# Kernel optimization log

Measured on AMD Instinct MI355X. Metric: run time of the kernel, lower is better.

Reference implementation:

```python
import jax, jax.numpy as jnp
import numpy as np

B, T, D, U, R = 64, 512, 256, 256, 4


def setup_inputs() -> dict:
    key = jax.random.key(0)
    ks = jax.random.split(key, 12)
    inputs = jax.random.normal(ks[0], (B, T, D), dtype=jnp.float32)
    # per-timestep dependency indices into past timesteps; must satisfy dep[t] <= t
    dependencies = jnp.minimum(
        jax.random.randint(ks[1], (T, R - 1), 0, T), jnp.arange(T)[:, None]
    ).astype(jnp.int32)
    mask = jax.random.randint(ks[2], (B, T), 0, 2).astype(jnp.int32)
    initial_states = jax.random.normal(ks[3], (R, B, U), dtype=jnp.float32) * 0.1
    s = 1.0 / np.sqrt(U)
    def w(k, shape):
        return jax.random.normal(k, shape, dtype=jnp.float32) * s
    return dict(
        inputs=inputs, dependencies=dependencies, mask=mask, initial_states=initial_states,
        Wz=w(ks[4], (D, U)), Wr=w(ks[5], (D, U)), Wh=w(ks[6], (D, U)),
        Uz=w(ks[7], (U, U)), Ur=w(ks[8], (U, U)), Uh=w(ks[9], (U, U)),
        bz=jnp.zeros((U,), jnp.float32), br=jnp.zeros((U,), jnp.float32), bh=jnp.zeros((U,), jnp.float32),
    )


def reference(inputs, dependencies, mask, initial_states, Wz, Wr, Wh, Uz, Ur, Uh, bz, br, bh):
    Bn, Tn, _ = inputs.shape
    Rn = initial_states.shape[0]
    Un = Uz.shape[0]

    x = jnp.swapaxes(inputs, 0, 1)              # [T, B, D]  (time_major swap)
    m = jnp.swapaxes(mask, 0, 1).astype(bool)   # [T, B]
    # dependencies[i] is consumed AFTER step i (sets states for step i+1) -> shift by one
    dep_in = jnp.concatenate(
        [jnp.zeros((1, dependencies.shape[1]), dependencies.dtype), dependencies[:-1]], axis=0
    )

    def cell(x_t, states):
        # states: [R, B, U]  (child-sum Graph-GRU over recurrent_size predecessor states)
        r = jax.nn.sigmoid(x_t @ Wr + states @ Ur + br)          # [R, B, U]
        h_sum = states.sum(0)                                    # [B, U]
        z = jax.nn.sigmoid(x_t @ Wz + h_sum @ Uz + bz)
        h_tilde = jnp.tanh(x_t @ Wh + (r * states).sum(0) @ Uh + bh)
        h = z * (h_sum / Rn) + (1.0 - z) * h_tilde
        return h  # GRU: output == new state

    def step(carry, xs):
        prev_out, prev_state, buf, t = carry
        x_t, m_t, dep_t = xs
        gathered = buf[dep_t]                                    # [R-1, B, U] irregular history gather
        cand = jnp.concatenate([prev_state[None], gathered], axis=0)
        states = jnp.where(t == 0, initial_states, cand)
        h = cell(x_t, states)
        mt = m_t[:, None]                                        # [B, 1]
        out_m = jnp.where(mt, h, prev_out)                       # masked output (pre_output carry)
        st_m = jnp.where(mt, h, prev_state)                      # masked state  (pre_states carry)
        buf = buf.at[t].set(st_m)                                # successive_states[t]
        return (out_m, st_m, buf, t + 1), out_m

    carry0 = (
        jnp.zeros((Bn, Un), inputs.dtype),
        jnp.zeros((Bn, Un), inputs.dtype),
        jnp.zeros((Tn, Bn, Un), inputs.dtype),
        jnp.array(0, jnp.int32),
    )
    (last_out, last_state, _, _), outs = jax.lax.scan(step, carry0, (x, m, dep_in))

    # zero_output_for_mask
    last_out = jnp.where(m[-1][:, None], last_out, jnp.zeros_like(last_out))
    outs = jnp.where(m[:, :, None], outs, jnp.zeros_like(outs))
    outputs = jnp.swapaxes(outs, 0, 1)                           # back to [B, T, U]
    return outputs, last_out, last_state
```

## Files before the change

### kernel.cpp

```cpp
#include <hip/hip_runtime.h>
#include <cstdint>
#include <cstddef>

#define BN 64
#define TN 512
#define DN 256
#define UN 256
#define NC 768
#define SLOTS (TN + 5)
#define ZSLOT (TN + 4)

__device__ __forceinline__ float sigm(float x) {
  return 1.0f / (1.0f + __expf(-x));
}
__device__ __forceinline__ float tanh_fast(float x) {
  float e = __expf(-2.0f * x);
  return 2.0f / (1.0f + e) - 1.0f;
}

__global__ __launch_bounds__(256) void build_wcat(
    const float* __restrict__ Wr, const float* __restrict__ Wz, const float* __restrict__ Wh,
    const float* __restrict__ br, const float* __restrict__ bz, const float* __restrict__ bh,
    float* __restrict__ wcat, float* __restrict__ bias)
{
  int idx = blockIdx.x * 256 + threadIdx.x;
  if (idx < DN * NC) {
    int k = idx / NC, c = idx % NC;
    float v;
    if (c < 256)      v = Wr[k * UN + c];
    else if (c < 512) v = Wz[k * UN + (c - 256)];
    else              v = Wh[k * UN + (c - 512)];
    wcat[idx] = v;
  }
  if (idx < NC) {
    bias[idx] = (idx < 256) ? br[idx] : ((idx < 512) ? bz[idx - 256] : bh[idx - 512]);
  }
}

__global__ __launch_bounds__(256) void gemm_xw(
    const float* __restrict__ X, const float* __restrict__ Wc,
    const float* __restrict__ bias, float* __restrict__ P)
{
  __shared__ float As[32][68];
  __shared__ float Bs[32][64];
  const int tid = threadIdx.x;
  const int m0 = blockIdx.x * 64;
  const int n0 = blockIdx.y * 64;
  const int ty = tid >> 4, tx = tid & 15;
  float acc[4][4] = {};

  const int ar = tid >> 3;
  const int ak = (tid & 7) * 4;
  const int bk = tid >> 4;
  const int bn = (tid & 15) * 4;

  for (int k0 = 0; k0 < DN; k0 += 32) {
    float4 a0 = *(const float4*)(X + (size_t)(m0 + ar) * DN + k0 + ak);
    float4 a1 = *(const float4*)(X + (size_t)(m0 + 32 + ar) * DN + k0 + ak);
    As[ak + 0][ar] = a0.x; As[ak + 1][ar] = a0.y; As[ak + 2][ar] = a0.z; As[ak + 3][ar] = a0.w;
    As[ak + 0][32 + ar] = a1.x; As[ak + 1][32 + ar] = a1.y; As[ak + 2][32 + ar] = a1.z; As[ak + 3][32 + ar] = a1.w;
    *(float4*)&Bs[bk][bn]      = *(const float4*)(Wc + (size_t)(k0 + bk) * NC + n0 + bn);
    *(float4*)&Bs[bk + 16][bn] = *(const float4*)(Wc + (size_t)(k0 + bk + 16) * NC + n0 + bn);
    __syncthreads();
#pragma unroll
    for (int kk = 0; kk < 32; kk++) {
      float4 av = *(const float4*)&As[kk][ty * 4];
      float4 bv = *(const float4*)&Bs[kk][tx * 4];
      acc[0][0] += av.x * bv.x; acc[0][1] += av.x * bv.y; acc[0][2] += av.x * bv.z; acc[0][3] += av.x * bv.w;
      acc[1][0] += av.y * bv.x; acc[1][1] += av.y * bv.y; acc[1][2] += av.y * bv.z; acc[1][3] += av.y * bv.w;
      acc[2][0] += av.z * bv.x; acc[2][1] += av.z * bv.y; acc[2][2] += av.z * bv.z; acc[2][3] += av.z * bv.w;
      acc[3][0] += av.w * bv.x; acc[3][1] += av.w * bv.y; acc[3][2] += av.w * bv.z; acc[3][3] += av.w * bv.w;
    }
    __syncthreads();
  }
  float4 bb = *(const float4*)(bias + n0 + tx * 4);
#pragma unroll
  for (int i = 0; i < 4; i++) {
    float4 o;
    o.x = acc[i][0] + bb.x; o.y = acc[i][1] + bb.y;
    o.z = acc[i][2] + bb.z; o.w = acc[i][3] + bb.w;
    *(float4*)(P + (size_t)(m0 + ty * 4 + i) * NC + n0 + tx * 4) = o;
  }
}

__global__ __launch_bounds__(1024, 4) void recurrent_kernel(
    const float* __restrict__ P,
    const float* __restrict__ Ur, const float* __restrict__ Uz, const float* __restrict__ Uh,
    const int* __restrict__ dep, const int* __restrict__ mask,
    const float* __restrict__ init,
    float* __restrict__ out,
    float* __restrict__ buf_s, float* __restrict__ buf_pr, float* __restrict__ buf_pz)
{
  const int b = blockIdx.x;
  const int tid = threadIdx.x;
  const int g = tid >> 8;
  const int u = tid & 255;
  const int qd = tid >> 6;
  const int cd = (tid & 63) * 4;

  float wh[64];
  {
    const float* p2 = Uh + (size_t)(64 * g) * UN + u;
#pragma unroll
    for (int kk = 0; kk < 64; kk++) {
      wh[kk] = p2[(size_t)kk * UN];
    }
  }

  __shared__ float ls[4][256], lpr[4][256], lpz[4][256];
  __shared__ float lx[NC];
  __shared__ float rs[256], hs[256], zv[256], hv[256];
  __shared__ float red0[4][256];
  __shared__ float reddR[16][256], reddZ[16][256];
  __shared__ float scur[256], prcur[256], pzcur[256];
  __shared__ int eff[TN];
  __shared__ int mloc[TN];
  __shared__ int deploc[TN * 3];

  for (int i = tid; i < TN; i += 1024) mloc[i] = mask[b * TN + i];
  for (int i = tid; i < TN * 3; i += 1024) deploc[i] = dep[i];

  const size_t bufBase = (size_t)b * SLOTS * UN;

  {
    float v = init[((size_t)g * BN + b) * UN + u];
    ls[g][u] = v;
    buf_s[bufBase + (size_t)(TN + g) * UN + u] = v;
    if (tid < 256) {
      scur[u] = 0.0f; prcur[u] = 0.0f; pzcur[u] = 0.0f;
      buf_s[bufBase + (size_t)ZSLOT * UN + u] = 0.0f;
      buf_pr[bufBase + (size_t)ZSLOT * UN + u] = 0.0f;
      buf_pz[bufBase + (size_t)ZSLOT * UN + u] = 0.0f;
    }
  }
  __syncthreads();

#pragma unroll 1
  for (int gg = 0; gg < 4; gg++) {
    float4 arA = {0, 0, 0, 0}, azA = {0, 0, 0, 0};
    const float* bR = Ur + (size_t)(qd * 16) * UN + cd;
    const float* bZ = Uz + (size_t)(qd * 16) * UN + cd;
#pragma unroll 4
    for (int kk = 0; kk < 16; kk++) {
      float hk = ls[gg][qd * 16 + kk];
      float4 w1 = *(const float4*)(bR + (size_t)kk * UN);
      float4 w2 = *(const float4*)(bZ + (size_t)kk * UN);
      arA.x = fmaf(hk, w1.x, arA.x); arA.y = fmaf(hk, w1.y, arA.y);
      arA.z = fmaf(hk, w1.z, arA.z); arA.w = fmaf(hk, w1.w, arA.w);
      azA.x = fmaf(hk, w2.x, azA.x); azA.y = fmaf(hk, w2.y, azA.y);
      azA.z = fmaf(hk, w2.z, azA.z); azA.w = fmaf(hk, w2.w, azA.w);
    }
    *(float4*)&reddR[qd][cd] = arA;
    *(float4*)&reddZ[qd][cd] = azA;
    __syncthreads();
    if (tid < 256) {
      float prn = 0.0f, pzn = 0.0f;
#pragma unroll
      for (int q = 0; q < 16; q++) { prn += reddR[q][tid]; pzn += reddZ[q][tid]; }
      buf_pr[bufBase + (size_t)(TN + gg) * UN + tid] = prn;
      buf_pz[bufBase + (size_t)(TN + gg) * UN + tid] = pzn;
    }
    __syncthreads();
  }

  const size_t outB = (size_t)b * TN * UN;
  const size_t pB = (size_t)b * TN * NC;

#pragma unroll 1
  for (int t = 0; t < TN; t++) {
    const int m = mloc[t];
    if (m == 0) {
      if (tid < 256) out[outB + (size_t)t * UN + u] = 0.0f;
      if (tid == 0) eff[t] = (t == 0) ? ZSLOT : eff[t - 1];
      __syncthreads();
      continue;
    }
    if (t > 0 && g == 0) {
      ls[0][u] = scur[u]; lpr[0][u] = prcur[u]; lpz[0][u] = pzcur[u];
    } else {
      int src = (t == 0) ? (TN + g) : eff[deploc[(t - 1) * 3 + (g - 1)]];
      size_t base = bufBase + (size_t)src * UN + u;
      ls[g][u]  = buf_s[base];
      lpr[g][u] = buf_pr[base];
      lpz[g][u] = buf_pz[base];
    }
    if (tid < NC) lx[tid] = P[pB + (size_t)t * NC + tid];
    __syncthreads();
    if (tid < 256) {
      float s0 = ls[0][u], s1 = ls[1][u], s2 = ls[2][u], s3 = ls[3][u];
      float xr = lx[u];
      float r0 = sigm(xr + lpr[0][u]);
      float r1 = sigm(xr + lpr[1][u]);
      float r2 = sigm(xr + lpr[2][u]);
      float r3 = sigm(xr + lpr[3][u]);
      rs[u] = r0 * s0 + r1 * s1 + r2 * s2 + r3 * s3;
      hs[u] = (s0 + s1) + (s2 + s3);
      zv[u] = sigm(lx[256 + u] + ((lpz[0][u] + lpz[1][u]) + (lpz[2][u] + lpz[3][u])));
    }
    __syncthreads();
    {
      float a0 = 0, a1 = 0, a2 = 0, a3 = 0;
      const float4* v4 = (const float4*)&rs[64 * g];
#pragma unroll
      for (int kk = 0; kk < 16; kk++) {
        float4 v = v4[kk];
        a0 += v.x * wh[4 * kk];     a1 += v.y * wh[4 * kk + 1];
        a2 += v.z * wh[4 * kk + 2]; a3 += v.w * wh[4 * kk + 3];
      }
      red0[g][u] = (a0 + a1) + (a2 + a3);
    }
    __syncthreads();
    if (tid < 256) {
      float ht = tanh_fast(lx[512 + u] + ((red0[0][u] + red0[1][u]) + (red0[2][u] + red0[3][u])));
      float z = zv[u];
      float h = z * hs[u] * 0.25f + (1.0f - z) * ht;
      hv[u] = h; scur[u] = h;
      out[outB + (size_t)t * UN + u] = h;
    }
    __syncthreads();
    {
      float4 arA = {0, 0, 0, 0}, azA = {0, 0, 0, 0};
      const float* bR = Ur + (size_t)(qd * 16) * UN + cd;
      const float* bZ = Uz + (size_t)(qd * 16) * UN + cd;
#pragma unroll 4
      for (int kk = 0; kk < 16; kk++) {
        float hk = hv[qd * 16 + kk];
        float4 w1 = *(const float4*)(bR + (size_t)kk * UN);
        float4 w2 = *(const float4*)(bZ + (size_t)kk * UN);
        arA.x = fmaf(hk, w1.x, arA.x); arA.y = fmaf(hk, w1.y, arA.y);
        arA.z = fmaf(hk, w1.z, arA.z); arA.w = fmaf(hk, w1.w, arA.w);
        azA.x = fmaf(hk, w2.x, azA.x); azA.y = fmaf(hk, w2.y, azA.y);
        azA.z = fmaf(hk, w2.z, azA.z); azA.w = fmaf(hk, w2.w, azA.w);
      }
      *(float4*)&reddR[qd][cd] = arA;
      *(float4*)&reddZ[qd][cd] = azA;
    }
    __syncthreads();
    if (tid < 256) {
      float prn = 0.0f, pzn = 0.0f;
#pragma unroll
      for (int q = 0; q < 16; q++) { prn += reddR[q][tid]; pzn += reddZ[q][tid]; }
      prcur[tid] = prn; pzcur[tid] = pzn;
      size_t base = bufBase + (size_t)t * UN + tid;
      buf_s[base]  = hv[tid];
      buf_pr[base] = prn;
      buf_pz[base] = pzn;
    }
    if (tid == 0) eff[t] = t;
    __syncthreads();
  }

  if (tid < 256) {
    float lst = scur[u];
    out[(size_t)BN * TN * UN + (size_t)b * UN + u] = mloc[TN - 1] ? lst : 0.0f;
    out[(size_t)BN * TN * UN + (size_t)BN * UN + (size_t)b * UN + u] = lst;
  }
}

extern "C" void kernel_launch(void* const* d_in, const int* in_sizes, int n_in,
                              void* d_out, int out_size, void* d_ws, size_t ws_size,
                              hipStream_t stream) {
  const float* inputs       = (const float*)d_in[0];
  const int*   dependencies = (const int*)d_in[1];
  const int*   mask         = (const int*)d_in[2];
  const float* initial      = (const float*)d_in[3];
  const float* Wz = (const float*)d_in[4];
  const float* Wr = (const float*)d_in[5];
  const float* Wh = (const float*)d_in[6];
  const float* Uz = (const float*)d_in[7];
  const float* Ur = (const float*)d_in[8];
  const float* Uh = (const float*)d_in[9];
  const float* bz = (const float*)d_in[10];
  const float* br = (const float*)d_in[11];
  const float* bh = (const float*)d_in[12];

  float* out = (float*)d_out;
  float* ws  = (float*)d_ws;
  float* wcat    = ws;
  float* bias    = wcat + (size_t)DN * NC;
  float* precomp = bias + NC;
  float* buf_s   = precomp + (size_t)BN * TN * NC;
  float* buf_pr  = buf_s + (size_t)BN * SLOTS * UN;
  float* buf_pz  = buf_pr + (size_t)BN * SLOTS * UN;

  build_wcat<<<(DN * NC + 255) / 256, 256, 0, stream>>>(Wr, Wz, Wh, br, bz, bh, wcat, bias);
  gemm_xw<<<dim3(BN * TN / 64, NC / 64), 256, 0, stream>>>(inputs, wcat, bias, precomp);
  recurrent_kernel<<<BN, 1024, 0, stream>>>(precomp, Ur, Uz, Uh, dependencies, mask, initial,
                                            out, buf_s, buf_pr, buf_pz);
}
```

Baseline: 2.062 ms.

## Halve recurrent block size and keep Ur/Uz slices in registers and LDS

Shrinks the recurrent kernel from 1024 to 512 threads and gives each thread twice as many Uh weights in registers. Part of each wave's Ur/Uz slice now lives in registers and part in shared memory, and only the remainder is streamed from global memory each step. The eff table is precomputed once by a single thread, so masked steps no longer need a barrier. This targets per-step global weight loads and barrier count, at the cost of much higher register pressure and fewer threads per step.

```diff
diff --git a/kernel.cpp b/kernel.cpp
--- a/kernel.cpp
+++ b/kernel.cpp
@@ -9,6 +9,11 @@
 #define NC 768
 #define SLOTS (TN + 5)
 #define ZSLOT (TN + 4)
+
+#define NT 512
+#define RREG 8
+#define RLDS 6
+#define RSTR 18
 
 __device__ __forceinline__ float sigm(float x) {
   return 1.0f / (1.0f + __expf(-x));
@@ -83,7 +88,7 @@
   }
 }
 
-__global__ __launch_bounds__(1024, 4) void recurrent_kernel(
+__global__ __launch_bounds__(NT, 2) void recurrent_kernel(
     const float* __restrict__ P,
     const float* __restrict__ Ur, const float* __restrict__ Uz, const float* __restrict__ Uh,
     const int* __restrict__ dep, const int* __restrict__ mask,
@@ -93,39 +98,65 @@
 {
   const int b = blockIdx.x;
   const int tid = threadIdx.x;
-  const int g = tid >> 8;
+  const int g2 = tid >> 8;
   const int u = tid & 255;
-  const int qd = tid >> 6;
-  const int cd = (tid & 63) * 4;
-
-  float wh[64];
+  const int wv = tid >> 6;
+  const int lane = tid & 63;
+  const int c4 = lane * 4;
+
+  float wh[128];
   {
-    const float* p2 = Uh + (size_t)(64 * g) * UN + u;
-#pragma unroll
-    for (int kk = 0; kk < 64; kk++) {
+    const float* p2 = Uh + (size_t)(128 * g2) * UN + u;
+#pragma unroll
+    for (int kk = 0; kk < 128; kk++) {
       wh[kk] = p2[(size_t)kk * UN];
     }
   }
-
+  float4 wrgR[RREG], wrgZ[RREG];
+  {
+    const float4* pR = (const float4*)Ur + (size_t)(32 * wv) * 64 + lane;
+    const float4* pZ = (const float4*)Uz + (size_t)(32 * wv) * 64 + lane;
+#pragma unroll
+    for (int r = 0; r < RREG; r++) {
+      wrgR[r] = pR[(size_t)r * 64];
+      wrgZ[r] = pZ[(size_t)r * 64];
+    }
+  }
+
+  __shared__ float4 wlds[2 * RLDS * 8 * 64];
   __shared__ float ls[4][256], lpr[4][256], lpz[4][256];
   __shared__ float lx[NC];
-  __shared__ float rs[256], hs[256], zv[256], hv[256];
-  __shared__ float red0[4][256];
-  __shared__ float reddR[16][256], reddZ[16][256];
+  __shared__ float rs[256], hs[256], zv[256];
+  __shared__ float red0[2][256];
+  __shared__ float redd2[2][8][256];
   __shared__ float scur[256], prcur[256], pzcur[256];
   __shared__ int eff[TN];
   __shared__ int mloc[TN];
   __shared__ int deploc[TN * 3];
 
-  for (int i = tid; i < TN; i += 1024) mloc[i] = mask[b * TN + i];
-  for (int i = tid; i < TN * 3; i += 1024) deploc[i] = dep[i];
+  {
+    const float4* pR = (const float4*)Ur + (size_t)(32 * wv + RREG) * 64 + lane;
+    const float4* pZ = (const float4*)Uz + (size_t)(32 * wv + RREG) * 64 + lane;
+#pragma unroll
+    for (int r = 0; r < RLDS; r++) {
+      wlds[((0 * RLDS + r) * 8 + wv) * 64 + lane] = pR[(size_t)r * 64];
+      wlds[((1 * RLDS + r) * 8 + wv) * 64 + lane] = pZ[(size_t)r * 64];
+    }
+  }
+
+  for (int i = tid; i < TN; i += NT) mloc[i] = mask[b * TN + i];
+  for (int i = tid; i < TN * 3; i += NT) deploc[i] = dep[i];
 
   const size_t bufBase = (size_t)b * SLOTS * UN;
 
   {
-    float v = init[((size_t)g * BN + b) * UN + u];
-    ls[g][u] = v;
-    buf_s[bufBase + (size_t)(TN + g) * UN + u] = v;
+#pragma unroll
+    for (int gi = 0; gi < 2; gi++) {
+      int gg = gi * 2 + g2;
+      float v = init[((size_t)gg * BN + b) * UN + u];
+      ls[gg][u] = v;
+      buf_s[bufBase + (size_t)(TN + gg) * UN + u] = v;
+    }
     if (tid < 256) {
       scur[u] = 0.0f; prcur[u] = 0.0f; pzcur[u] = 0.0f;
       buf_s[bufBase + (size_t)ZSLOT * UN + u] = 0.0f;
@@ -135,28 +166,56 @@
   }
   __syncthreads();
 
+  if (tid == 0) {
+    int e = ZSLOT;
+    for (int t2 = 0; t2 < TN; t2++) { if (mloc[t2]) e = t2; eff[t2] = e; }
+  }
+
+  auto proj2 = [&](const float* hsrc) {
+    float4 aR = {0, 0, 0, 0}, aZ = {0, 0, 0, 0};
+    const float* hb = hsrc + 32 * wv;
+#pragma unroll
+    for (int r = 0; r < RREG; r++) {
+      float hk = hb[r];
+      aR.x = fmaf(hk, wrgR[r].x, aR.x); aR.y = fmaf(hk, wrgR[r].y, aR.y);
+      aR.z = fmaf(hk, wrgR[r].z, aR.z); aR.w = fmaf(hk, wrgR[r].w, aR.w);
+      aZ.x = fmaf(hk, wrgZ[r].x, aZ.x); aZ.y = fmaf(hk, wrgZ[r].y, aZ.y);
+      aZ.z = fmaf(hk, wrgZ[r].z, aZ.z); aZ.w = fmaf(hk, wrgZ[r].w, aZ.w);
+    }
+#pragma unroll
+    for (int r = 0; r < RLDS; r++) {
+      float hk = hb[RREG + r];
+      float4 w0 = wlds[((0 * RLDS + r) * 8 + wv) * 64 + lane];
+      float4 w1 = wlds[((1 * RLDS + r) * 8 + wv) * 64 + lane];
+      aR.x = fmaf(hk, w0.x, aR.x); aR.y = fmaf(hk, w0.y, aR.y);
+      aR.z = fmaf(hk, w0.z, aR.z); aR.w = fmaf(hk, w0.w, aR.w);
+      aZ.x = fmaf(hk, w1.x, aZ.x); aZ.y = fmaf(hk, w1.y, aZ.y);
+      aZ.z = fmaf(hk, w1.z, aZ.z); aZ.w = fmaf(hk, w1.w, aZ.w);
+    }
+    const float4* pR = (const float4*)Ur + (size_t)(32 * wv + RREG + RLDS) * 64 + lane;
+    const float4* pZ = (const float4*)Uz + (size_t)(32 * wv + RREG + RLDS) * 64 + lane;
+#pragma unroll 6
+    for (int r = 0; r < RSTR; r++) {
+      float hk = hb[RREG + RLDS + r];
+      float4 w0 = pR[(size_t)r * 64];
+      float4 w1 = pZ[(size_t)r * 64];
+      aR.x = fmaf(hk, w0.x, aR.x); aR.y = fmaf(hk, w0.y, aR.y);
+      aR.z = fmaf(hk, w0.z, aR.z); aR.w = fmaf(hk, w0.w, aR.w);
+      aZ.x = fmaf(hk, w1.x, aZ.x); aZ.y = fmaf(hk, w1.y, aZ.y);
+      aZ.z = fmaf(hk, w1.z, aZ.z); aZ.w = fmaf(hk, w1.w, aZ.w);
+    }
+    *(float4*)&redd2[0][wv][c4] = aR;
+    *(float4*)&redd2[1][wv][c4] = aZ;
+  };
+
 #pragma unroll 1
   for (int gg = 0; gg < 4; gg++) {
-    float4 arA = {0, 0, 0, 0}, azA = {0, 0, 0, 0};
-    const float* bR = Ur + (size_t)(qd * 16) * UN + cd;
-    const float* bZ = Uz + (size_t)(qd * 16) * UN + cd;
-#pragma unroll 4
-    for (int kk = 0; kk < 16; kk++) {
-      float hk = ls[gg][qd * 16 + kk];
-      float4 w1 = *(const float4*)(bR + (size_t)kk * UN);
-      float4 w2 = *(const float4*)(bZ + (size_t)kk * UN);
-      arA.x = fmaf(hk, w1.x, arA.x); arA.y = fmaf(hk, w1.y, arA.y);
-      arA.z = fmaf(hk, w1.z, arA.z); arA.w = fmaf(hk, w1.w, arA.w);
-      azA.x = fmaf(hk, w2.x, azA.x); azA.y = fmaf(hk, w2.y, azA.y);
-      azA.z = fmaf(hk, w2.z, azA.z); azA.w = fmaf(hk, w2.w, azA.w);
-    }
-    *(float4*)&reddR[qd][cd] = arA;
-    *(float4*)&reddZ[qd][cd] = azA;
+    proj2(ls[gg]);
     __syncthreads();
     if (tid < 256) {
       float prn = 0.0f, pzn = 0.0f;
 #pragma unroll
-      for (int q = 0; q < 16; q++) { prn += reddR[q][tid]; pzn += reddZ[q][tid]; }
+      for (int q = 0; q < 8; q++) { prn += redd2[0][q][tid]; pzn += redd2[1][q][tid]; }
       buf_pr[bufBase + (size_t)(TN + gg) * UN + tid] = prn;
       buf_pz[bufBase + (size_t)(TN + gg) * UN + tid] = pzn;
     }
@@ -171,20 +230,22 @@
     const int m = mloc[t];
     if (m == 0) {
       if (tid < 256) out[outB + (size_t)t * UN + u] = 0.0f;
-      if (tid == 0) eff[t] = (t == 0) ? ZSLOT : eff[t - 1];
-      __syncthreads();
       continue;
     }
-    if (t > 0 && g == 0) {
-      ls[0][u] = scur[u]; lpr[0][u] = prcur[u]; lpz[0][u] = pzcur[u];
-    } else {
-      int src = (t == 0) ? (TN + g) : eff[deploc[(t - 1) * 3 + (g - 1)]];
-      size_t base = bufBase + (size_t)src * UN + u;
-      ls[g][u]  = buf_s[base];
-      lpr[g][u] = buf_pr[base];
-      lpz[g][u] = buf_pz[base];
-    }
-    if (tid < NC) lx[tid] = P[pB + (size_t)t * NC + tid];
+#pragma unroll
+    for (int gi = 0; gi < 2; gi++) {
+      int gg = gi * 2 + g2;
+      if (t > 0 && gg == 0) {
+        ls[0][u] = scur[u]; lpr[0][u] = prcur[u]; lpz[0][u] = pzcur[u];
+      } else {
+        int src = (t == 0) ? (TN + gg) : eff[deploc[(t - 1) * 3 + (gg - 1)]];
+        size_t base = bufBase + (size_t)src * UN + u;
+        ls[gg][u]  = buf_s[base];
+        lpr[gg][u] = buf_pr[base];
+        lpz[gg][u] = buf_pz[base];
+      }
+    }
+    for (int i = tid; i < NC; i += NT) lx[i] = P[pB + (size_t)t * NC + i];
     __syncthreads();
     if (tid < 256) {
       float s0 = ls[0][u], s1 = ls[1][u], s2 = ls[2][u], s3 = ls[3][u];
@@ -200,53 +261,36 @@
     __syncthreads();
     {
       float a0 = 0, a1 = 0, a2 = 0, a3 = 0;
-      const float4* v4 = (const float4*)&rs[64 * g];
-#pragma unroll
-      for (int kk = 0; kk < 16; kk++) {
+      const float4* v4 = (const float4*)&rs[128 * g2];
+#pragma unroll
+      for (int kk = 0; kk < 32; kk++) {
         float4 v = v4[kk];
         a0 += v.x * wh[4 * kk];     a1 += v.y * wh[4 * kk + 1];
         a2 += v.z * wh[4 * kk + 2]; a3 += v.w * wh[4 * kk + 3];
       }
-      red0[g][u] = (a0 + a1) + (a2 + a3);
-    }
-    __syncthreads();
-    if (tid < 256) {
-      float ht = tanh_fast(lx[512 + u] + ((red0[0][u] + red0[1][u]) + (red0[2][u] + red0[3][u])));
+      red0[g2][u] = (a0 + a1) + (a2 + a3);
+    }
+    __syncthreads();
+    if (tid < 256) {
+      float ht = tanh_fast(lx[512 + u] + (red0[0][u] + red0[1][u]));
       float z = zv[u];
       float h = z * hs[u] * 0.25f + (1.0f - z) * ht;
-      hv[u] = h; scur[u] = h;
+      scur[u] = h;
       out[outB + (size_t)t * UN + u] = h;
     }
     __syncthreads();
-    {
-      float4 arA = {0, 0, 0, 0}, azA = {0, 0, 0, 0};
-      const float* bR = Ur + (size_t)(qd * 16) * UN + cd;
-      const float* bZ = Uz + (size_t)(qd * 16) * UN + cd;
-#pragma unroll 4
-      for (int kk = 0; kk < 16; kk++) {
-        float hk = hv[qd * 16 + kk];
-        float4 w1 = *(const float4*)(bR + (size_t)kk * UN);
-        float4 w2 = *(const float4*)(bZ + (size_t)kk * UN);
-        arA.x = fmaf(hk, w1.x, arA.x); arA.y = fmaf(hk, w1.y, arA.y);
-        arA.z = fmaf(hk, w1.z, arA.z); arA.w = fmaf(hk, w1.w, arA.w);
-        azA.x = fmaf(hk, w2.x, azA.x); azA.y = fmaf(hk, w2.y, azA.y);
-        azA.z = fmaf(hk, w2.z, azA.z); azA.w = fmaf(hk, w2.w, azA.w);
-      }
-      *(float4*)&reddR[qd][cd] = arA;
-      *(float4*)&reddZ[qd][cd] = azA;
-    }
+    proj2(scur);
     __syncthreads();
     if (tid < 256) {
       float prn = 0.0f, pzn = 0.0f;
 #pragma unroll
-      for (int q = 0; q < 16; q++) { prn += reddR[q][tid]; pzn += reddZ[q][tid]; }
+      for (int q = 0; q < 8; q++) { prn += redd2[0][q][tid]; pzn += redd2[1][q][tid]; }
       prcur[tid] = prn; pzcur[tid] = pzn;
       size_t base = bufBase + (size_t)t * UN + tid;
-      buf_s[base]  = hv[tid];
+      buf_s[base]  = scur[tid];
       buf_pr[base] = prn;
       buf_pz[base] = pzn;
     }
-    if (tid == 0) eff[t] = t;
     __syncthreads();
   }
 
@@ -285,6 +329,6 @@
 
   build_wcat<<<(DN * NC + 255) / 256, 256, 0, stream>>>(Wr, Wz, Wh, br, bz, bh, wcat, bias);
   gemm_xw<<<dim3(BN * TN / 64, NC / 64), 256, 0, stream>>>(inputs, wcat, bias, precomp);
-  recurrent_kernel<<<BN, 1024, 0, stream>>>(precomp, Ur, Uz, Uh, dependencies, mask, initial,
-                                            out, buf_s, buf_pr, buf_pz);
-}
+  recurrent_kernel<<<BN, NT, 0, stream>>>(precomp, Ur, Uz, Uh, dependencies, mask, initial,
+                                          out, buf_s, buf_pr, buf_pz);
+}
```

Measured after the change: 2.184 ms. 1.06x slower.

## Split each batch recurrence across four cooperating blocks with global flag sync

Applied to the files above, without the earlier changes.

The recurrent kernel now uses four 512-thread blocks per batch element, each owning a 64-column slice of the hidden state. Its slice of Ur/Uz is kept in shared memory instead of being re-read from global memory every step. The blocks swap their r*s and h slices through global memory using release/acquire flags and spin-waits, twice per active timestep. Masked-out steps now skip all work and barriers, and the effective-slot table is precomputed. This spreads work over more CUs and cuts global weight traffic, at the cost of cross-block synchronisation latency and a reliance on all 256 blocks being co-resident to avoid deadlock.

```diff
diff --git a/kernel.cpp b/kernel.cpp
--- a/kernel.cpp
+++ b/kernel.cpp
@@ -9,6 +9,8 @@
 #define NC 768
 #define SLOTS (TN + 5)
 #define ZSLOT (TN + 4)
+#define JW 4
+#define NT 512
 
 __device__ __forceinline__ float sigm(float x) {
   return 1.0f / (1.0f + __expf(-x));
@@ -21,7 +23,8 @@
 __global__ __launch_bounds__(256) void build_wcat(
     const float* __restrict__ Wr, const float* __restrict__ Wz, const float* __restrict__ Wh,
     const float* __restrict__ br, const float* __restrict__ bz, const float* __restrict__ bh,
-    float* __restrict__ wcat, float* __restrict__ bias)
+    float* __restrict__ wcat, float* __restrict__ bias,
+    int* __restrict__ flagA, int* __restrict__ flagB)
 {
   int idx = blockIdx.x * 256 + threadIdx.x;
   if (idx < DN * NC) {
@@ -35,6 +38,7 @@
   if (idx < NC) {
     bias[idx] = (idx < 256) ? br[idx] : ((idx < 512) ? bz[idx - 256] : bh[idx - 512]);
   }
+  if (idx < BN * JW) { flagA[idx] = 0; flagB[idx] = 0; }
 }
 
 __global__ __launch_bounds__(256) void gemm_xw(
@@ -83,177 +87,218 @@
   }
 }
 
-__global__ __launch_bounds__(1024, 4) void recurrent_kernel(
+__global__ __launch_bounds__(NT, 1) void recurrent_kernel(
     const float* __restrict__ P,
     const float* __restrict__ Ur, const float* __restrict__ Uz, const float* __restrict__ Uh,
     const int* __restrict__ dep, const int* __restrict__ mask,
     const float* __restrict__ init,
     float* __restrict__ out,
-    float* __restrict__ buf_s, float* __restrict__ buf_pr, float* __restrict__ buf_pz)
+    float* __restrict__ buf_s, float* __restrict__ buf_pr, float* __restrict__ buf_pz,
+    float* __restrict__ xrs, int* flagA, int* flagB)
 {
-  const int b = blockIdx.x;
+  const int bj = blockIdx.x;
+  const int b = bj & (BN - 1);
+  const int j = bj >> 6;
+  const int col0 = j * 64;
   const int tid = threadIdx.x;
-  const int g = tid >> 8;
-  const int u = tid & 255;
-  const int qd = tid >> 6;
-  const int cd = (tid & 63) * 4;
-
-  float wh[64];
+  const int c = tid & 63;
+
+  const int kg8 = tid >> 6;
+  float wh[32];
   {
-    const float* p2 = Uh + (size_t)(64 * g) * UN + u;
-#pragma unroll
-    for (int kk = 0; kk < 64; kk++) {
-      wh[kk] = p2[(size_t)kk * UN];
-    }
-  }
-
-  __shared__ float ls[4][256], lpr[4][256], lpz[4][256];
-  __shared__ float lx[NC];
-  __shared__ float rs[256], hs[256], zv[256], hv[256];
-  __shared__ float red0[4][256];
-  __shared__ float reddR[16][256], reddZ[16][256];
-  __shared__ float scur[256], prcur[256], pzcur[256];
+    const float* pu = Uh + (size_t)(32 * kg8) * UN + col0 + c;
+#pragma unroll
+    for (int kk = 0; kk < 32; kk++) wh[kk] = pu[(size_t)kk * UN];
+  }
+
+  __shared__ float4 wrz[2][256][16];
+  __shared__ float hfull[256];
+  __shared__ float rfull[256];
+  __shared__ float ls[4][64], lpr[4][64], lpz[4][64];
+  __shared__ float lx[3][64];
+  __shared__ float rsl[64], hsl[64], zvl[64];
+  __shared__ float redB[8][64];
+  __shared__ float redd[2][16][64];
+  __shared__ float scur[64], prcur[64], pzcur[64];
   __shared__ int eff[TN];
   __shared__ int mloc[TN];
   __shared__ int deploc[TN * 3];
 
-  for (int i = tid; i < TN; i += 1024) mloc[i] = mask[b * TN + i];
-  for (int i = tid; i < TN * 3; i += 1024) deploc[i] = dep[i];
-
-  const size_t bufBase = (size_t)b * SLOTS * UN;
-
-  {
-    float v = init[((size_t)g * BN + b) * UN + u];
-    ls[g][u] = v;
-    buf_s[bufBase + (size_t)(TN + g) * UN + u] = v;
-    if (tid < 256) {
-      scur[u] = 0.0f; prcur[u] = 0.0f; pzcur[u] = 0.0f;
-      buf_s[bufBase + (size_t)ZSLOT * UN + u] = 0.0f;
-      buf_pr[bufBase + (size_t)ZSLOT * UN + u] = 0.0f;
-      buf_pz[bufBase + (size_t)ZSLOT * UN + u] = 0.0f;
-    }
-  }
+  for (int i = tid; i < 2 * 256 * 16; i += NT) {
+    int mat = i >> 12, k = (i >> 4) & 255, ch = i & 15;
+    const float* src = mat ? Uz : Ur;
+    wrz[mat][k][ch] = *(const float4*)(src + (size_t)k * UN + col0 + ch * 4);
+  }
+  for (int i = tid; i < TN; i += NT) mloc[i] = mask[b * TN + i];
+  for (int i = tid; i < TN * 3; i += NT) deploc[i] = dep[i];
+  if (tid < 64) { scur[c] = 0.0f; prcur[c] = 0.0f; pzcur[c] = 0.0f; }
   __syncthreads();
+
+  if (tid == 0) {
+    int e = ZSLOT;
+    for (int t2 = 0; t2 < TN; t2++) { if (mloc[t2]) e = t2; eff[t2] = e; }
+  }
+
+  const size_t bufS = (size_t)b * SLOTS * UN;
+  const size_t bufP = (size_t)(b * JW + j) * SLOTS * 64;
 
 #pragma unroll 1
   for (int gg = 0; gg < 4; gg++) {
-    float4 arA = {0, 0, 0, 0}, azA = {0, 0, 0, 0};
-    const float* bR = Ur + (size_t)(qd * 16) * UN + cd;
-    const float* bZ = Uz + (size_t)(qd * 16) * UN + cd;
-#pragma unroll 4
-    for (int kk = 0; kk < 16; kk++) {
-      float hk = ls[gg][qd * 16 + kk];
-      float4 w1 = *(const float4*)(bR + (size_t)kk * UN);
-      float4 w2 = *(const float4*)(bZ + (size_t)kk * UN);
-      arA.x = fmaf(hk, w1.x, arA.x); arA.y = fmaf(hk, w1.y, arA.y);
-      arA.z = fmaf(hk, w1.z, arA.z); arA.w = fmaf(hk, w1.w, arA.w);
-      azA.x = fmaf(hk, w2.x, azA.x); azA.y = fmaf(hk, w2.y, azA.y);
-      azA.z = fmaf(hk, w2.z, azA.z); azA.w = fmaf(hk, w2.w, azA.w);
-    }
-    *(float4*)&reddR[qd][cd] = arA;
-    *(float4*)&reddZ[qd][cd] = azA;
-    __syncthreads();
-    if (tid < 256) {
-      float prn = 0.0f, pzn = 0.0f;
-#pragma unroll
-      for (int q = 0; q < 16; q++) { prn += reddR[q][tid]; pzn += reddZ[q][tid]; }
-      buf_pr[bufBase + (size_t)(TN + gg) * UN + tid] = prn;
-      buf_pz[bufBase + (size_t)(TN + gg) * UN + tid] = pzn;
-    }
-    __syncthreads();
-  }
+    if (tid < 256) hfull[tid] = init[((size_t)gg * BN + b) * UN + tid];
+    __syncthreads();
+    {
+      int mat = tid >> 8, kg16 = (tid >> 4) & 15, ch = tid & 15;
+      float4 a = {0, 0, 0, 0};
+#pragma unroll
+      for (int kk = 0; kk < 16; kk++) {
+        int k = kg16 * 16 + kk;
+        float hk = hfull[k];
+        float4 w = wrz[mat][k][ch];
+        a.x = fmaf(hk, w.x, a.x); a.y = fmaf(hk, w.y, a.y);
+        a.z = fmaf(hk, w.z, a.z); a.w = fmaf(hk, w.w, a.w);
+      }
+      *(float4*)&redd[mat][kg16][ch * 4] = a;
+    }
+    __syncthreads();
+    if (tid < 128) {
+      int mat = tid >> 6;
+      float s = 0.0f;
+#pragma unroll
+      for (int q = 0; q < 16; q++) s += redd[mat][q][c];
+      if (mat == 0) buf_pr[bufP + (size_t)(TN + gg) * 64 + c] = s;
+      else          buf_pz[bufP + (size_t)(TN + gg) * 64 + c] = s;
+    }
+    if (tid < 64) buf_s[bufS + (size_t)(TN + gg) * UN + col0 + c] = hfull[col0 + c];
+    __syncthreads();
+  }
+  if (tid < 64) {
+    buf_s[bufS + (size_t)ZSLOT * UN + col0 + c] = 0.0f;
+    buf_pr[bufP + (size_t)ZSLOT * 64 + c] = 0.0f;
+    buf_pz[bufP + (size_t)ZSLOT * 64 + c] = 0.0f;
+  }
+  __syncthreads();
 
   const size_t outB = (size_t)b * TN * UN;
   const size_t pB = (size_t)b * TN * NC;
+  const int fbase = b * JW;
+  int na = 0;
 
 #pragma unroll 1
   for (int t = 0; t < TN; t++) {
-    const int m = mloc[t];
-    if (m == 0) {
-      if (tid < 256) out[outB + (size_t)t * UN + u] = 0.0f;
-      if (tid == 0) eff[t] = (t == 0) ? ZSLOT : eff[t - 1];
-      __syncthreads();
+    if (mloc[t] == 0) {
+      if (tid < 64) out[outB + (size_t)t * UN + col0 + c] = 0.0f;
       continue;
     }
-    if (t > 0 && g == 0) {
-      ls[0][u] = scur[u]; lpr[0][u] = prcur[u]; lpz[0][u] = pzcur[u];
-    } else {
-      int src = (t == 0) ? (TN + g) : eff[deploc[(t - 1) * 3 + (g - 1)]];
-      size_t base = bufBase + (size_t)src * UN + u;
-      ls[g][u]  = buf_s[base];
-      lpr[g][u] = buf_pr[base];
-      lpz[g][u] = buf_pz[base];
-    }
-    if (tid < NC) lx[tid] = P[pB + (size_t)t * NC + tid];
+    na++;
+    for (int i = tid; i < 960; i += NT) {
+      if (i < 256) {
+        int g = i >> 6, cc = i & 63;
+        int src = (t == 0) ? (TN + g) : ((g == 0) ? -1 : eff[deploc[(t - 1) * 3 + (g - 1)]]);
+        ls[g][cc] = (src < 0) ? scur[cc] : buf_s[bufS + (size_t)src * UN + col0 + cc];
+      } else if (i < 768) {
+        int i2 = i - 256;
+        int arr = i2 >> 8, g = (i2 >> 6) & 3, cc = i2 & 63;
+        int src = (t == 0) ? (TN + g) : ((g == 0) ? -1 : eff[deploc[(t - 1) * 3 + (g - 1)]]);
+        if (arr == 0) lpr[g][cc] = (src < 0) ? prcur[cc] : buf_pr[bufP + (size_t)src * 64 + cc];
+        else          lpz[g][cc] = (src < 0) ? pzcur[cc] : buf_pz[bufP + (size_t)src * 64 + cc];
+      } else {
+        int i2 = i - 768;
+        int sel = i2 >> 6, cc = i2 & 63;
+        lx[sel][cc] = P[pB + (size_t)t * NC + sel * UN + col0 + cc];
+      }
+    }
+    __syncthreads();
+    if (tid < 64) {
+      float s0 = ls[0][c], s1 = ls[1][c], s2 = ls[2][c], s3 = ls[3][c];
+      float xr = lx[0][c];
+      float rsv = sigm(xr + lpr[0][c]) * s0 + sigm(xr + lpr[1][c]) * s1
+                + sigm(xr + lpr[2][c]) * s2 + sigm(xr + lpr[3][c]) * s3;
+      rsl[c] = rsv;
+      hsl[c] = (s0 + s1) + (s2 + s3);
+      zvl[c] = sigm(lx[1][c] + ((lpz[0][c] + lpz[1][c]) + (lpz[2][c] + lpz[3][c])));
+      xrs[(size_t)(fbase + j) * 64 + c] = rsv;
+      __threadfence();
+    }
+    __syncthreads();
+    if (tid == 0)
+      __hip_atomic_store(&flagB[fbase + j], na, __ATOMIC_RELEASE, __HIP_MEMORY_SCOPE_AGENT);
+    if (tid < JW - 1) {
+      int jj = tid + (tid >= j ? 1 : 0);
+      while (__hip_atomic_load(&flagB[fbase + jj], __ATOMIC_ACQUIRE, __HIP_MEMORY_SCOPE_AGENT) < na)
+        __builtin_amdgcn_s_sleep(1);
+    }
     __syncthreads();
     if (tid < 256) {
-      float s0 = ls[0][u], s1 = ls[1][u], s2 = ls[2][u], s3 = ls[3][u];
-      float xr = lx[u];
-      float r0 = sigm(xr + lpr[0][u]);
-      float r1 = sigm(xr + lpr[1][u]);
-      float r2 = sigm(xr + lpr[2][u]);
-      float r3 = sigm(xr + lpr[3][u]);
-      rs[u] = r0 * s0 + r1 * s1 + r2 * s2 + r3 * s3;
-      hs[u] = (s0 + s1) + (s2 + s3);
-      zv[u] = sigm(lx[256 + u] + ((lpz[0][u] + lpz[1][u]) + (lpz[2][u] + lpz[3][u])));
+      int jj = tid >> 6;
+      rfull[tid] = (jj == j) ? rsl[c]
+        : __hip_atomic_load(&xrs[(size_t)(fbase + jj) * 64 + (tid & 63)],
+                            __ATOMIC_RELAXED, __HIP_MEMORY_SCOPE_AGENT);
     }
     __syncthreads();
     {
-      float a0 = 0, a1 = 0, a2 = 0, a3 = 0;
-      const float4* v4 = (const float4*)&rs[64 * g];
+      float a = 0.0f;
+#pragma unroll
+      for (int kk = 0; kk < 32; kk++) a = fmaf(rfull[32 * kg8 + kk], wh[kk], a);
+      redB[kg8][c] = a;
+    }
+    __syncthreads();
+    if (tid < 64) {
+      float hb = 0.0f;
+#pragma unroll
+      for (int q = 0; q < 8; q++) hb += redB[q][c];
+      float ht = tanh_fast(lx[2][c] + hb);
+      float z = zvl[c];
+      float h = z * hsl[c] * 0.25f + (1.0f - z) * ht;
+      scur[c] = h;
+      out[outB + (size_t)t * UN + col0 + c] = h;
+      buf_s[bufS + (size_t)t * UN + col0 + c] = h;
+      __threadfence();
+    }
+    __syncthreads();
+    if (tid == 0)
+      __hip_atomic_store(&flagA[fbase + j], na, __ATOMIC_RELEASE, __HIP_MEMORY_SCOPE_AGENT);
+    if (tid < JW - 1) {
+      int jj = tid + (tid >= j ? 1 : 0);
+      while (__hip_atomic_load(&flagA[fbase + jj], __ATOMIC_ACQUIRE, __HIP_MEMORY_SCOPE_AGENT) < na)
+        __builtin_amdgcn_s_sleep(1);
+    }
+    __syncthreads();
+    if (tid < 256) {
+      int jj = tid >> 6;
+      hfull[tid] = (jj == j) ? scur[c]
+        : __hip_atomic_load(&buf_s[bufS + (size_t)t * UN + tid],
+                            __ATOMIC_RELAXED, __HIP_MEMORY_SCOPE_AGENT);
+    }
+    __syncthreads();
+    {
+      int mat = tid >> 8, kg16 = (tid >> 4) & 15, ch = tid & 15;
+      float4 a = {0, 0, 0, 0};
 #pragma unroll
       for (int kk = 0; kk < 16; kk++) {
-        float4 v = v4[kk];
-        a0 += v.x * wh[4 * kk];     a1 += v.y * wh[4 * kk + 1];
-        a2 += v.z * wh[4 * kk + 2]; a3 += v.w * wh[4 * kk + 3];
+        int k = kg16 * 16 + kk;
+        float hk = hfull[k];
+        float4 w = wrz[mat][k][ch];
+        a.x = fmaf(hk, w.x, a.x); a.y = fmaf(hk, w.y, a.y);
+        a.z = fmaf(hk, w.z, a.z); a.w = fmaf(hk, w.w, a.w);
       }
-      red0[g][u] = (a0 + a1) + (a2 + a3);
-    }
-    __syncthreads();
-    if (tid < 256) {
-      float ht = tanh_fast(lx[512 + u] + ((red0[0][u] + red0[1][u]) + (red0[2][u] + red0[3][u])));
-      float z = zv[u];
-      float h = z * hs[u] * 0.25f + (1.0f - z) * ht;
-      hv[u] = h; scur[u] = h;
-      out[outB + (size_t)t * UN + u] = h;
-    }
-    __syncthreads();
-    {
-      float4 arA = {0, 0, 0, 0}, azA = {0, 0, 0, 0};
-      const float* bR = Ur + (size_t)(qd * 16) * UN + cd;
-      const float* bZ = Uz + (size_t)(qd * 16) * UN + cd;
-#pragma unroll 4
-      for (int kk = 0; kk < 16; kk++) {
-        float hk = hv[qd * 16 + kk];
-        float4 w1 = *(const float4*)(bR + (size_t)kk * UN);
-        float4 w2 = *(const float4*)(bZ + (size_t)kk * UN);
-        arA.x = fmaf(hk, w1.x, arA.x); arA.y = fmaf(hk, w1.y, arA.y);
-        arA.z = fmaf(hk, w1.z, arA.z); arA.w = fmaf(hk, w1.w, arA.w);
-        azA.x = fmaf(hk, w2.x, azA.x); azA.y = fmaf(hk, w2.y, azA.y);
-        azA.z = fmaf(hk, w2.z, azA.z); azA.w = fmaf(hk, w2.w, azA.w);
-      }
-      *(float4*)&reddR[qd][cd] = arA;
-      *(float4*)&reddZ[qd][cd] = azA;
-    }
-    __syncthreads();
-    if (tid < 256) {
-      float prn = 0.0f, pzn = 0.0f;
-#pragma unroll
-      for (int q = 0; q < 16; q++) { prn += reddR[q][tid]; pzn += reddZ[q][tid]; }
-      prcur[tid] = prn; pzcur[tid] = pzn;
-      size_t base = bufBase + (size_t)t * UN + tid;
-      buf_s[base]  = hv[tid];
-      buf_pr[base] = prn;
-      buf_pz[base] = pzn;
-    }
-    if (tid == 0) eff[t] = t;
-    __syncthreads();
-  }
-
-  if (tid < 256) {
-    float lst = scur[u];
-    out[(size_t)BN * TN * UN + (size_t)b * UN + u] = mloc[TN - 1] ? lst : 0.0f;
-    out[(size_t)BN * TN * UN + (size_t)BN * UN + (size_t)b * UN + u] = lst;
+      *(float4*)&redd[mat][kg16][ch * 4] = a;
+    }
+    __syncthreads();
+    if (tid < 128) {
+      int mat = tid >> 6;
+      float s = 0.0f;
+#pragma unroll
+      for (int q = 0; q < 16; q++) s += redd[mat][q][c];
+      if (mat == 0) { prcur[c] = s; buf_pr[bufP + (size_t)t * 64 + c] = s; }
+      else          { pzcur[c] = s; buf_pz[bufP + (size_t)t * 64 + c] = s; }
+    }
+    __syncthreads();
+  }
+
+  if (tid < 64) {
+    float lst = scur[c];
+    out[(size_t)BN * TN * UN + (size_t)b * UN + col0 + c] = mloc[TN - 1] ? lst : 0.0f;
+    out[(size_t)BN * TN * UN + (size_t)BN * UN + (size_t)b * UN + col0 + c] = lst;
   }
 }
 
@@ -281,10 +326,14 @@
   float* precomp = bias + NC;
   float* buf_s   = precomp + (size_t)BN * TN * NC;
   float* buf_pr  = buf_s + (size_t)BN * SLOTS * UN;
-  float* buf_pz  = buf_pr + (size_t)BN * SLOTS * UN;
-
-  build_wcat<<<(DN * NC + 255) / 256, 256, 0, stream>>>(Wr, Wz, Wh, br, bz, bh, wcat, bias);
+  float* buf_pz  = buf_pr + (size_t)BN * JW * SLOTS * 64;
+  float* xrs     = buf_pz + (size_t)BN * JW * SLOTS * 64;
+  int*   flagA   = (int*)(xrs + (size_t)BN * JW * 64);
+  int*   flagB   = flagA + BN * JW;
+
+  build_wcat<<<(DN * NC + 255) / 256, 256, 0, stream>>>(Wr, Wz, Wh, br, bz, bh, wcat, bias,
+                                                        flagA, flagB);
   gemm_xw<<<dim3(BN * TN / 64, NC / 64), 256, 0, stream>>>(inputs, wcat, bias, precomp);
-  recurrent_kernel<<<BN, 1024, 0, stream>>>(precomp, Ur, Uz, Uh, dependencies, mask, initial,
-                                            out, buf_s, buf_pr, buf_pz);
-}
+  recurrent_kernel<<<BN * JW, NT, 0, stream>>>(precomp, Ur, Uz, Uh, dependencies, mask, initial,
+                                               out, buf_s, buf_pr, buf_pz, xrs, flagA, flagB);
+}
```

New measurement: 5.329 ms. 2.58x slower.

## Prefetch next active step's states and cache recurrent weights in LDS/registers

Applied to the files above, without the earlier changes.

Precomputes the effective-slot and next-active-step tables up front, so masked steps no longer need a barrier. While the current step's Uh matvec runs, it issues global loads for the next active step's gathered states and input projections. It also restructures the Ur/Uz projection so each wave handles one matrix over 32 rows, with part of the weights held in LDS, part in registers and the rest streamed. The goal is to take global-load latency and extra barriers off the sequential critical path, at the cost of more LDS, higher register pressure and more complex state handoff logic.

```diff
diff --git a/kernel.cpp b/kernel.cpp
--- a/kernel.cpp
+++ b/kernel.cpp
@@ -9,6 +9,10 @@
 #define NC 768
 #define SLOTS (TN + 5)
 #define ZSLOT (TN + 4)
+
+#define WROWS_LDS 6
+#define WROWS_REG 2
+#define WROWS_STR 24
 
 __device__ __forceinline__ float sigm(float x) {
   return 1.0f / (1.0f + __expf(-x));
@@ -83,7 +87,7 @@
   }
 }
 
-__global__ __launch_bounds__(1024, 4) void recurrent_kernel(
+__global__ __launch_bounds__(1024, 1) void recurrent_kernel(
     const float* __restrict__ P,
     const float* __restrict__ Ur, const float* __restrict__ Uz, const float* __restrict__ Uh,
     const int* __restrict__ dep, const int* __restrict__ mask,
@@ -93,39 +97,50 @@
 {
   const int b = blockIdx.x;
   const int tid = threadIdx.x;
-  const int g = tid >> 8;
-  const int u = tid & 255;
-  const int qd = tid >> 6;
-  const int cd = (tid & 63) * 4;
+  const int g4 = tid >> 8;
+  const int u  = tid & 255;
+  const int wv = tid >> 6;
+  const int mat = wv & 1;
+  const int s   = wv >> 1;
+  const int l   = tid & 63;
 
   float wh[64];
   {
-    const float* p2 = Uh + (size_t)(64 * g) * UN + u;
-#pragma unroll
-    for (int kk = 0; kk < 64; kk++) {
-      wh[kk] = p2[(size_t)kk * UN];
-    }
-  }
-
+    const float* pu = Uh + (size_t)(64 * g4) * UN + u;
+#pragma unroll
+    for (int kk = 0; kk < 64; kk++) wh[kk] = pu[(size_t)kk * UN];
+  }
+  const float* Um = mat ? Uz : Ur;
+  float4 wrg0 = ((const float4*)Um)[(size_t)(32 * s + WROWS_LDS + 0) * 64 + l];
+  float4 wrg1 = ((const float4*)Um)[(size_t)(32 * s + WROWS_LDS + 1) * 64 + l];
+
+  __shared__ float4 wlds4[2][8][WROWS_LDS][64];
   __shared__ float ls[4][256], lpr[4][256], lpz[4][256];
-  __shared__ float lx[NC];
-  __shared__ float rs[256], hs[256], zv[256], hv[256];
+  __shared__ float lxf[NC];
+  __shared__ float rs[256], hs[256], zv[256];
   __shared__ float red0[4][256];
-  __shared__ float reddR[16][256], reddZ[16][256];
+  __shared__ float redd[2][8][256];
   __shared__ float scur[256], prcur[256], pzcur[256];
-  __shared__ int eff[TN];
-  __shared__ int mloc[TN];
+  __shared__ int eff[TN], nxt[TN], mloc[TN];
   __shared__ int deploc[TN * 3];
 
+  for (int i = tid; i < 2 * 8 * WROWS_LDS * 64; i += 1024) {
+    int mm = i / (8 * WROWS_LDS * 64);
+    int r2 = i % (8 * WROWS_LDS * 64);
+    int ss = r2 / (WROWS_LDS * 64);
+    int rr = (r2 / 64) % WROWS_LDS;
+    int ll = i & 63;
+    wlds4[mm][ss][rr][ll] = ((const float4*)(mm ? Uz : Ur))[(size_t)(32 * ss + rr) * 64 + ll];
+  }
   for (int i = tid; i < TN; i += 1024) mloc[i] = mask[b * TN + i];
   for (int i = tid; i < TN * 3; i += 1024) deploc[i] = dep[i];
 
   const size_t bufBase = (size_t)b * SLOTS * UN;
 
   {
-    float v = init[((size_t)g * BN + b) * UN + u];
-    ls[g][u] = v;
-    buf_s[bufBase + (size_t)(TN + g) * UN + u] = v;
+    float v = init[((size_t)g4 * BN + b) * UN + u];
+    ls[g4][u] = v;
+    buf_s[bufBase + (size_t)(TN + g4) * UN + u] = v;
     if (tid < 256) {
       scur[u] = 0.0f; prcur[u] = 0.0f; pzcur[u] = 0.0f;
       buf_s[bufBase + (size_t)ZSLOT * UN + u] = 0.0f;
@@ -135,119 +150,147 @@
   }
   __syncthreads();
 
+  if (tid == 0) {
+    int e = ZSLOT;
+    for (int t2 = 0; t2 < TN; t2++) { if (mloc[t2]) e = t2; eff[t2] = e; }
+  } else if (tid == 64) {
+    int e = TN;
+    for (int t2 = TN - 1; t2 >= 0; t2--) { if (mloc[t2]) e = t2; nxt[t2] = e; }
+  }
+
+  auto projD = [&](const float* hsrc) {
+    const float* hb = hsrc + 32 * s;
+    float4 a = {0, 0, 0, 0};
+#pragma unroll
+    for (int r = 0; r < WROWS_LDS; r++) {
+      float hk = hb[r];
+      float4 w = wlds4[mat][s][r][l];
+      a.x = fmaf(hk, w.x, a.x); a.y = fmaf(hk, w.y, a.y);
+      a.z = fmaf(hk, w.z, a.z); a.w = fmaf(hk, w.w, a.w);
+    }
+    {
+      float hk = hb[WROWS_LDS + 0];
+      a.x = fmaf(hk, wrg0.x, a.x); a.y = fmaf(hk, wrg0.y, a.y);
+      a.z = fmaf(hk, wrg0.z, a.z); a.w = fmaf(hk, wrg0.w, a.w);
+    }
+    {
+      float hk = hb[WROWS_LDS + 1];
+      a.x = fmaf(hk, wrg1.x, a.x); a.y = fmaf(hk, wrg1.y, a.y);
+      a.z = fmaf(hk, wrg1.z, a.z); a.w = fmaf(hk, wrg1.w, a.w);
+    }
+    const float4* p = (const float4*)Um + (size_t)(32 * s + WROWS_LDS + WROWS_REG) * 64 + l;
+#pragma unroll 8
+    for (int kk = 0; kk < WROWS_STR; kk++) {
+      float hk = hb[WROWS_LDS + WROWS_REG + kk];
+      float4 w = p[(size_t)kk * 64];
+      a.x = fmaf(hk, w.x, a.x); a.y = fmaf(hk, w.y, a.y);
+      a.z = fmaf(hk, w.z, a.z); a.w = fmaf(hk, w.w, a.w);
+    }
+    *(float4*)&redd[mat][s][4 * l] = a;
+  };
+
 #pragma unroll 1
   for (int gg = 0; gg < 4; gg++) {
-    float4 arA = {0, 0, 0, 0}, azA = {0, 0, 0, 0};
-    const float* bR = Ur + (size_t)(qd * 16) * UN + cd;
-    const float* bZ = Uz + (size_t)(qd * 16) * UN + cd;
-#pragma unroll 4
-    for (int kk = 0; kk < 16; kk++) {
-      float hk = ls[gg][qd * 16 + kk];
-      float4 w1 = *(const float4*)(bR + (size_t)kk * UN);
-      float4 w2 = *(const float4*)(bZ + (size_t)kk * UN);
-      arA.x = fmaf(hk, w1.x, arA.x); arA.y = fmaf(hk, w1.y, arA.y);
-      arA.z = fmaf(hk, w1.z, arA.z); arA.w = fmaf(hk, w1.w, arA.w);
-      azA.x = fmaf(hk, w2.x, azA.x); azA.y = fmaf(hk, w2.y, azA.y);
-      azA.z = fmaf(hk, w2.z, azA.z); azA.w = fmaf(hk, w2.w, azA.w);
-    }
-    *(float4*)&reddR[qd][cd] = arA;
-    *(float4*)&reddZ[qd][cd] = azA;
-    __syncthreads();
-    if (tid < 256) {
-      float prn = 0.0f, pzn = 0.0f;
-#pragma unroll
-      for (int q = 0; q < 16; q++) { prn += reddR[q][tid]; pzn += reddZ[q][tid]; }
-      buf_pr[bufBase + (size_t)(TN + gg) * UN + tid] = prn;
-      buf_pz[bufBase + (size_t)(TN + gg) * UN + tid] = pzn;
+    projD(&ls[gg][0]);
+    __syncthreads();
+    if (tid < 512) {
+      int mm = tid >> 8, c = tid & 255;
+      float v = 0.0f;
+#pragma unroll
+      for (int q = 0; q < 8; q++) v += redd[mm][q][c];
+      (mm ? buf_pz : buf_pr)[bufBase + (size_t)(TN + gg) * UN + c] = v;
     }
     __syncthreads();
   }
 
   const size_t outB = (size_t)b * TN * UN;
   const size_t pB = (size_t)b * TN * NC;
+  bool havePre = false;
+  float eLs = 0.0f, eLpr = 0.0f, eLpz = 0.0f, eLx = 0.0f;
+  int eSrc = -2;
 
 #pragma unroll 1
   for (int t = 0; t < TN; t++) {
-    const int m = mloc[t];
-    if (m == 0) {
+    if (mloc[t] == 0) {
       if (tid < 256) out[outB + (size_t)t * UN + u] = 0.0f;
-      if (tid == 0) eff[t] = (t == 0) ? ZSLOT : eff[t - 1];
-      __syncthreads();
       continue;
     }
-    if (t > 0 && g == 0) {
-      ls[0][u] = scur[u]; lpr[0][u] = prcur[u]; lpz[0][u] = pzcur[u];
-    } else {
-      int src = (t == 0) ? (TN + g) : eff[deploc[(t - 1) * 3 + (g - 1)]];
-      size_t base = bufBase + (size_t)src * UN + u;
-      ls[g][u]  = buf_s[base];
-      lpr[g][u] = buf_pr[base];
-      lpz[g][u] = buf_pz[base];
-    }
-    if (tid < NC) lx[tid] = P[pB + (size_t)t * NC + tid];
+    if (!havePre) {
+      if (t > 0 && g4 == 0) {
+        ls[0][u] = scur[u]; lpr[0][u] = prcur[u]; lpz[0][u] = pzcur[u];
+      } else {
+        int src = (t == 0) ? (TN + g4) : eff[deploc[(t - 1) * 3 + (g4 - 1)]];
+        size_t base = bufBase + (size_t)src * UN + u;
+        ls[g4][u]  = buf_s[base];
+        lpr[g4][u] = buf_pr[base];
+        lpz[g4][u] = buf_pz[base];
+      }
+      if (tid < NC) lxf[tid] = P[pB + (size_t)t * NC + tid];
+    }
     __syncthreads();
     if (tid < 256) {
       float s0 = ls[0][u], s1 = ls[1][u], s2 = ls[2][u], s3 = ls[3][u];
-      float xr = lx[u];
-      float r0 = sigm(xr + lpr[0][u]);
-      float r1 = sigm(xr + lpr[1][u]);
-      float r2 = sigm(xr + lpr[2][u]);
-      float r3 = sigm(xr + lpr[3][u]);
-      rs[u] = r0 * s0 + r1 * s1 + r2 * s2 + r3 * s3;
+      float xr = lxf[u];
+      rs[u] = sigm(xr + lpr[0][u]) * s0 + sigm(xr + lpr[1][u]) * s1
+            + sigm(xr + lpr[2][u]) * s2 + sigm(xr + lpr[3][u]) * s3;
       hs[u] = (s0 + s1) + (s2 + s3);
-      zv[u] = sigm(lx[256 + u] + ((lpz[0][u] + lpz[1][u]) + (lpz[2][u] + lpz[3][u])));
-    }
-    __syncthreads();
+      zv[u] = sigm(lxf[256 + u] + ((lpz[0][u] + lpz[1][u]) + (lpz[2][u] + lpz[3][u])));
+    }
+    __syncthreads();
+    const int tn = (t + 1 < TN) ? nxt[t + 1] : TN;
+    if (tn < TN) {
+      if (g4 > 0) {
+        eSrc = eff[deploc[(tn - 1) * 3 + (g4 - 1)]];
+        if (eSrc != t) {
+          size_t base = bufBase + (size_t)eSrc * UN + u;
+          eLs = buf_s[base]; eLpr = buf_pr[base]; eLpz = buf_pz[base];
+        }
+      }
+      if (tid < NC) eLx = P[pB + (size_t)tn * NC + tid];
+    }
     {
       float a0 = 0, a1 = 0, a2 = 0, a3 = 0;
-      const float4* v4 = (const float4*)&rs[64 * g];
+      const float4* v4 = (const float4*)&rs[64 * g4];
 #pragma unroll
       for (int kk = 0; kk < 16; kk++) {
         float4 v = v4[kk];
         a0 += v.x * wh[4 * kk];     a1 += v.y * wh[4 * kk + 1];
         a2 += v.z * wh[4 * kk + 2]; a3 += v.w * wh[4 * kk + 3];
       }
-      red0[g][u] = (a0 + a1) + (a2 + a3);
+      red0[g4][u] = (a0 + a1) + (a2 + a3);
     }
     __syncthreads();
     if (tid < 256) {
-      float ht = tanh_fast(lx[512 + u] + ((red0[0][u] + red0[1][u]) + (red0[2][u] + red0[3][u])));
+      float ht = tanh_fast(lxf[512 + u] + ((red0[0][u] + red0[1][u]) + (red0[2][u] + red0[3][u])));
       float z = zv[u];
       float h = z * hs[u] * 0.25f + (1.0f - z) * ht;
-      hv[u] = h; scur[u] = h;
+      scur[u] = h;
       out[outB + (size_t)t * UN + u] = h;
-    }
-    __syncthreads();
-    {
-      float4 arA = {0, 0, 0, 0}, azA = {0, 0, 0, 0};
-      const float* bR = Ur + (size_t)(qd * 16) * UN + cd;
-      const float* bZ = Uz + (size_t)(qd * 16) * UN + cd;
-#pragma unroll 4
-      for (int kk = 0; kk < 16; kk++) {
-        float hk = hv[qd * 16 + kk];
-        float4 w1 = *(const float4*)(bR + (size_t)kk * UN);
-        float4 w2 = *(const float4*)(bZ + (size_t)kk * UN);
-        arA.x = fmaf(hk, w1.x, arA.x); arA.y = fmaf(hk, w1.y, arA.y);
-        arA.z = fmaf(hk, w1.z, arA.z); arA.w = fmaf(hk, w1.w, arA.w);
-        azA.x = fmaf(hk, w2.x, azA.x); azA.y = fmaf(hk, w2.y, azA.y);
-        azA.z = fmaf(hk, w2.z, azA.z); azA.w = fmaf(hk, w2.w, azA.w);
-      }
-      *(float4*)&reddR[qd][cd] = arA;
-      *(float4*)&reddZ[qd][cd] = azA;
-    }
+      buf_s[bufBase + (size_t)t * UN + u] = h;
+    }
+    __syncthreads();
+    projD(scur);
     __syncthreads();
     if (tid < 256) {
       float prn = 0.0f, pzn = 0.0f;
 #pragma unroll
-      for (int q = 0; q < 16; q++) { prn += reddR[q][tid]; pzn += reddZ[q][tid]; }
-      prcur[tid] = prn; pzcur[tid] = pzn;
-      size_t base = bufBase + (size_t)t * UN + tid;
-      buf_s[base]  = hv[tid];
-      buf_pr[base] = prn;
-      buf_pz[base] = pzn;
-    }
-    if (tid == 0) eff[t] = t;
-    __syncthreads();
+      for (int q = 0; q < 8; q++) { prn += redd[0][q][u]; pzn += redd[1][q][u]; }
+      prcur[u] = prn; pzcur[u] = pzn;
+      buf_pr[bufBase + (size_t)t * UN + u] = prn;
+      buf_pz[bufBase + (size_t)t * UN + u] = pzn;
+      if (tn < TN) { ls[0][u] = scur[u]; lpr[0][u] = prn; lpz[0][u] = pzn; }
+    } else if (tn < TN) {
+      if (eSrc == t) {
+        float prn = 0.0f, pzn = 0.0f;
+#pragma unroll
+        for (int q = 0; q < 8; q++) { prn += redd[0][q][u]; pzn += redd[1][q][u]; }
+        ls[g4][u] = scur[u]; lpr[g4][u] = prn; lpz[g4][u] = pzn;
+      } else {
+        ls[g4][u] = eLs; lpr[g4][u] = eLpr; lpz[g4][u] = eLpz;
+      }
+    }
+    if (tn < TN && tid < NC) lxf[tid] = eLx;
+    havePre = (tn < TN);
   }
 
   if (tid < 256) {
```

Result: slower. 2.210 ms (+7.2%).
